# Kernel optimization log

Hardware: AMD Instinct MI355X
Metric: run time of the kernel (lower is better)

## Reference

```python
import jax, jax.numpy as jnp
import numpy as np

EPS_NORM = 1e-12  # torch F.normalize eps
CLAMP_MIN = 1e-6

def _l2_normalize(x, axis):
    n = jnp.sqrt(jnp.sum(x * x, axis=axis, keepdims=True))
    return x / jnp.maximum(n, EPS_NORM)

def setup_inputs() -> dict:
    key = jax.random.key(0)
    k1, k2 = jax.random.split(key)
    embedding = jax.random.normal(k1, (384,), dtype=jnp.float32)
    corpus_embeddings = jax.random.normal(k2, (1000000, 384), dtype=jnp.float32)
    return {"embedding": embedding, "corpus_embeddings": corpus_embeddings, "k": 5}

def reference(embedding, corpus_embeddings, k):
    # embedding: [d] -> [1, d]; corpus_embeddings: [N, d]
    e = embedding[None, :] if embedding.ndim == 1 else embedding
    e = _l2_normalize(e, axis=1)                      # [1, d]
    c = _l2_normalize(corpus_embeddings, axis=1)      # [N, d]
    # cosine_similarity of already-unit vectors == dot product (re-normalization
    # inside torch cosine_similarity is a no-op on unit vectors)
    sims = jnp.einsum('nd,d->n', c, e[0])             # [N]
    sims = jnp.maximum(sims, CLAMP_MIN)               # torch.clamp(min=1e-6)
    sims = jnp.nan_to_num(sims, nan=0.0)
    k = min(int(k), sims.shape[0])
    top_k_similarities, top_k_indices = jax.lax.top_k(sims, k)
    return top_k_similarities, top_k_indices
```

## Files before the change

### kernel.cpp

```cpp
#include <hip/hip_runtime.h>
#include <math.h>

#define NBLK 1024
#define K 5
#define D 384
#define D4 (D/4)
#define THREADS 256
#define GROUPS_PER_BLOCK (THREADS/16)
#define C1 (GROUPS_PER_BLOCK*K)
#define C2 (NBLK*K)

__device__ __forceinline__ bool better(float v1, int r1, float v2, int r2) {
    return (v1 > v2) || (v1 == v2 && r1 < r2);
}

__global__ void qnorm_kernel(const float* __restrict__ q, float* __restrict__ invq) {
    int l = threadIdx.x;
    float ss = 0.f;
    #pragma unroll
    for (int j = 0; j < 6; ++j) {
        float x = q[l + 64*j];
        ss += x * x;
    }
    #pragma unroll
    for (int m = 1; m < 64; m <<= 1) ss += __shfl_xor(ss, m);
    if (l == 0) invq[0] = 1.0f / fmaxf(sqrtf(ss), 1e-12f);
}

__global__ __launch_bounds__(THREADS) void sim_topk_kernel(
        const float* __restrict__ corpus, const float* __restrict__ q,
        const float* __restrict__ invq_p,
        float* __restrict__ bVals, int* __restrict__ bIdx, int N) {
    __shared__ float qs[D];
    float invq = invq_p[0];
    for (int i = threadIdx.x; i < D; i += THREADS) qs[i] = q[i] * invq;
    __syncthreads();
    const float4* q4 = reinterpret_cast<const float4*>(qs);

    const int lane16 = threadIdx.x & 15;
    const int group  = threadIdx.x >> 4;
    const int ggid   = blockIdx.x * GROUPS_PER_BLOCK + group;
    const int gcount = gridDim.x * GROUPS_PER_BLOCK;

    float tv[K]; int ti[K];
    #pragma unroll
    for (int i = 0; i < K; ++i) { tv[i] = -INFINITY; ti[i] = 0x7fffffff; }

    for (int row = ggid; row < N; row += gcount) {
        const float4* r4 = reinterpret_cast<const float4*>(corpus + (size_t)row * D);
        float dot = 0.f, nrm = 0.f;
        #pragma unroll
        for (int j = 0; j < 6; ++j) {
            float4 x = r4[lane16 + 16*j];
            float4 w = q4[lane16 + 16*j];
            dot += x.x*w.x + x.y*w.y + x.z*w.z + x.w*w.w;
            nrm += x.x*x.x + x.y*x.y + x.z*x.z + x.w*x.w;
        }
        #pragma unroll
        for (int m = 1; m < 16; m <<= 1) {
            dot += __shfl_xor(dot, m);
            nrm += __shfl_xor(nrm, m);
        }
        if (lane16 == 0) {
            float sim = dot / fmaxf(sqrtf(nrm), 1e-12f);
            sim = fmaxf(sim, 1e-6f);
            if (sim != sim) sim = 0.f;
            if (sim > tv[K-1]) {
                int j = K - 1;
                while (j > 0 && tv[j-1] < sim) { tv[j] = tv[j-1]; ti[j] = ti[j-1]; --j; }
                tv[j] = sim; ti[j] = row;
            }
        }
    }

    __shared__ float cv[C1]; __shared__ int ci[C1];
    __shared__ float rv[THREADS]; __shared__ int ri[THREADS]; __shared__ int rs[THREADS];
    if (lane16 == 0) {
        #pragma unroll
        for (int i = 0; i < K; ++i) { cv[group*K + i] = tv[i]; ci[group*K + i] = ti[i]; }
    }
    __syncthreads();

    for (int r = 0; r < K; ++r) {
        float bv = -INFINITY; int bi = 0x7fffffff; int bslot = -1;
        for (int c = threadIdx.x; c < C1; c += THREADS)
            if (better(cv[c], ci[c], bv, bi)) { bv = cv[c]; bi = ci[c]; bslot = c; }
        rv[threadIdx.x] = bv; ri[threadIdx.x] = bi; rs[threadIdx.x] = bslot;
        __syncthreads();
        for (int s = THREADS/2; s > 0; s >>= 1) {
            if (threadIdx.x < s) {
                if (better(rv[threadIdx.x+s], ri[threadIdx.x+s], rv[threadIdx.x], ri[threadIdx.x])) {
                    rv[threadIdx.x] = rv[threadIdx.x+s];
                    ri[threadIdx.x] = ri[threadIdx.x+s];
                    rs[threadIdx.x] = rs[threadIdx.x+s];
                }
            }
            __syncthreads();
        }
        if (threadIdx.x == 0) {
            bVals[blockIdx.x*K + r] = rv[0];
            bIdx [blockIdx.x*K + r] = ri[0];
            if (rs[0] >= 0) cv[rs[0]] = -INFINITY;
        }
        __syncthreads();
    }
}

__global__ __launch_bounds__(THREADS) void final_topk_kernel(
        const float* __restrict__ bVals, const int* __restrict__ bIdx,
        float* __restrict__ out, int nC) {
    __shared__ float cv[C2]; __shared__ int ci[C2];
    __shared__ float rv[THREADS]; __shared__ int ri[THREADS]; __shared__ int rs[THREADS];
    for (int c = threadIdx.x; c < nC; c += THREADS) { cv[c] = bVals[c]; ci[c] = bIdx[c]; }
    __syncthreads();

    for (int r = 0; r < K; ++r) {
        float bv = -INFINITY; int bi = 0x7fffffff; int bslot = -1;
        for (int c = threadIdx.x; c < nC; c += THREADS)
            if (better(cv[c], ci[c], bv, bi)) { bv = cv[c]; bi = ci[c]; bslot = c; }
        rv[threadIdx.x] = bv; ri[threadIdx.x] = bi; rs[threadIdx.x] = bslot;
        __syncthreads();
        for (int s = THREADS/2; s > 0; s >>= 1) {
            if (threadIdx.x < s) {
                if (better(rv[threadIdx.x+s], ri[threadIdx.x+s], rv[threadIdx.x], ri[threadIdx.x])) {
                    rv[threadIdx.x] = rv[threadIdx.x+s];
                    ri[threadIdx.x] = ri[threadIdx.x+s];
                    rs[threadIdx.x] = rs[threadIdx.x+s];
                }
            }
            __syncthreads();
        }
        if (threadIdx.x == 0) {
            out[r]     = rv[0];
            out[K + r] = (float)ri[0];
            if (rs[0] >= 0) cv[rs[0]] = -INFINITY;
        }
        __syncthreads();
    }
}

extern "C" void kernel_launch(void* const* d_in, const int* in_sizes, int n_in,
                              void* d_out, int out_size, void* d_ws, size_t ws_size,
                              hipStream_t stream) {
    const float* q      = (const float*)d_in[0];
    const float* corpus = (const float*)d_in[1];
    const int N = in_sizes[1] / D;

    char* ws = (char*)d_ws;
    float* invq  = (float*)ws;
    float* bVals = (float*)(ws + 256);
    int*   bIdx  = (int*)  (ws + 256 + NBLK*K*4);

    float* out = (float*)d_out;

    qnorm_kernel<<<1, 64, 0, stream>>>(q, invq);
    sim_topk_kernel<<<NBLK, THREADS, 0, stream>>>(corpus, q, invq, bVals, bIdx, N);
    final_topk_kernel<<<1, THREADS, 0, stream>>>(bVals, bIdx, out, NBLK*K);
}
```

Measured before the change: 289.8 us.

## Fuse query norm, similarity and final top-k into one kernel with last-block reduction

Result: slower. 513.6 us (+77.2%).

```diff
diff --git a/kernel.cpp b/kernel.cpp
--- a/kernel.cpp
+++ b/kernel.cpp
@@ -4,7 +4,6 @@
 #define NBLK 1024
 #define K 5
 #define D 384
-#define D4 (D/4)
 #define THREADS 256
 #define GROUPS_PER_BLOCK (THREADS/16)
 #define C1 (GROUPS_PER_BLOCK*K)
@@ -14,67 +13,107 @@
     return (v1 > v2) || (v1 == v2 && r1 < r2);
 }
 
-__global__ void qnorm_kernel(const float* __restrict__ q, float* __restrict__ invq) {
-    int l = threadIdx.x;
-    float ss = 0.f;
-    #pragma unroll
-    for (int j = 0; j < 6; ++j) {
-        float x = q[l + 64*j];
-        ss += x * x;
-    }
-    #pragma unroll
-    for (int m = 1; m < 64; m <<= 1) ss += __shfl_xor(ss, m);
-    if (l == 0) invq[0] = 1.0f / fmaxf(sqrtf(ss), 1e-12f);
-}
-
-__global__ __launch_bounds__(THREADS) void sim_topk_kernel(
+__global__ __launch_bounds__(THREADS) void fused_sim_topk_kernel(
         const float* __restrict__ corpus, const float* __restrict__ q,
-        const float* __restrict__ invq_p,
-        float* __restrict__ bVals, int* __restrict__ bIdx, int N) {
+        float* __restrict__ bVals, int* __restrict__ bIdx,
+        unsigned int* __restrict__ counter,
+        float* __restrict__ out, int N) {
     __shared__ float qs[D];
-    float invq = invq_p[0];
-    for (int i = threadIdx.x; i < D; i += THREADS) qs[i] = q[i] * invq;
-    __syncthreads();
-    const float4* q4 = reinterpret_cast<const float4*>(qs);
+    __shared__ float s_invq;
+    __shared__ float cv[C1]; __shared__ int ci[C1];
+    __shared__ float rv[THREADS]; __shared__ int ri[THREADS]; __shared__ int rs[THREADS];
+    __shared__ bool amLast;
+
+    float4* qs4 = (float4*)qs;
+    if (threadIdx.x < D/4) qs4[threadIdx.x] = ((const float4*)q)[threadIdx.x];
+    __syncthreads();
+    if (threadIdx.x < 64) {
+        float ss = 0.f;
+        #pragma unroll
+        for (int j = 0; j < 6; ++j) { float x = qs[threadIdx.x + 64*j]; ss += x*x; }
+        #pragma unroll
+        for (int m = 1; m < 64; m <<= 1) ss += __shfl_xor(ss, m);
+        if (threadIdx.x == 0) s_invq = 1.0f / fmaxf(sqrtf(ss), 1e-12f);
+    }
+    __syncthreads();
+    if (threadIdx.x < D/4) {
+        float iv = s_invq;
+        float4 v = qs4[threadIdx.x];
+        v.x *= iv; v.y *= iv; v.z *= iv; v.w *= iv;
+        qs4[threadIdx.x] = v;
+    }
+    __syncthreads();
+    const float4* q4 = (const float4*)qs;
 
     const int lane16 = threadIdx.x & 15;
     const int group  = threadIdx.x >> 4;
     const int ggid   = blockIdx.x * GROUPS_PER_BLOCK + group;
-    const int gcount = gridDim.x * GROUPS_PER_BLOCK;
+    const int gcount = NBLK * GROUPS_PER_BLOCK;
 
     float tv[K]; int ti[K];
     #pragma unroll
     for (int i = 0; i < K; ++i) { tv[i] = -INFINITY; ti[i] = 0x7fffffff; }
 
-    for (int row = ggid; row < N; row += gcount) {
-        const float4* r4 = reinterpret_cast<const float4*>(corpus + (size_t)row * D);
+    auto insert = [&](float sim, int r) {
+        if (sim > tv[K-1]) {
+            int j = K - 1;
+            while (j > 0 && tv[j-1] < sim) { tv[j] = tv[j-1]; ti[j] = ti[j-1]; --j; }
+            tv[j] = sim; ti[j] = r;
+        }
+    };
+
+    int row = ggid;
+    for (; row + gcount < N; row += 2*gcount) {
+        const int rowB = row + gcount;
+        const float4* rA = (const float4*)(corpus + (size_t)row  * D);
+        const float4* rB = (const float4*)(corpus + (size_t)rowB * D);
+        float dotA = 0.f, nrmA = 0.f, dotB = 0.f, nrmB = 0.f;
+        #pragma unroll
+        for (int j = 0; j < 6; ++j) {
+            float4 w  = q4[lane16 + 16*j];
+            float4 xA = rA[lane16 + 16*j];
+            float4 xB = rB[lane16 + 16*j];
+            dotA += xA.x*w.x + xA.y*w.y + xA.z*w.z + xA.w*w.w;
+            nrmA += xA.x*xA.x + xA.y*xA.y + xA.z*xA.z + xA.w*xA.w;
+            dotB += xB.x*w.x + xB.y*w.y + xB.z*w.z + xB.w*w.w;
+            nrmB += xB.x*xB.x + xB.y*xB.y + xB.z*xB.z + xB.w*xB.w;
+        }
+        #pragma unroll
+        for (int m = 1; m < 16; m <<= 1) {
+            dotA += __shfl_xor(dotA, m); nrmA += __shfl_xor(nrmA, m);
+            dotB += __shfl_xor(dotB, m); nrmB += __shfl_xor(nrmB, m);
+        }
+        if (lane16 == 0) {
+            float simA = dotA / fmaxf(sqrtf(nrmA), 1e-12f);
+            simA = fmaxf(simA, 1e-6f);
+            if (simA != simA) simA = 0.f;
+            insert(simA, row);
+            float simB = dotB / fmaxf(sqrtf(nrmB), 1e-12f);
+            simB = fmaxf(simB, 1e-6f);
+            if (simB != simB) simB = 0.f;
+            insert(simB, rowB);
+        }
+    }
+    if (row < N) {
+        const float4* rA = (const float4*)(corpus + (size_t)row * D);
         float dot = 0.f, nrm = 0.f;
         #pragma unroll
         for (int j = 0; j < 6; ++j) {
-            float4 x = r4[lane16 + 16*j];
             float4 w = q4[lane16 + 16*j];
+            float4 x = rA[lane16 + 16*j];
             dot += x.x*w.x + x.y*w.y + x.z*w.z + x.w*w.w;
             nrm += x.x*x.x + x.y*x.y + x.z*x.z + x.w*x.w;
         }
         #pragma unroll
-        for (int m = 1; m < 16; m <<= 1) {
-            dot += __shfl_xor(dot, m);
-            nrm += __shfl_xor(nrm, m);
-        }
+        for (int m = 1; m < 16; m <<= 1) { dot += __shfl_xor(dot, m); nrm += __shfl_xor(nrm, m); }
         if (lane16 == 0) {
             float sim = dot / fmaxf(sqrtf(nrm), 1e-12f);
             sim = fmaxf(sim, 1e-6f);
             if (sim != sim) sim = 0.f;
-            if (sim > tv[K-1]) {
-                int j = K - 1;
-                while (j > 0 && tv[j-1] < sim) { tv[j] = tv[j-1]; ti[j] = ti[j-1]; --j; }
-                tv[j] = sim; ti[j] = row;
-            }
-        }
-    }
-
-    __shared__ float cv[C1]; __shared__ int ci[C1];
-    __shared__ float rv[THREADS]; __shared__ int ri[THREADS]; __shared__ int rs[THREADS];
+            insert(sim, row);
+        }
+    }
+
     if (lane16 == 0) {
         #pragma unroll
         for (int i = 0; i < K; ++i) { cv[group*K + i] = tv[i]; ci[group*K + i] = ti[i]; }
@@ -104,20 +143,22 @@
         }
         __syncthreads();
     }
-}
-
-__global__ __launch_bounds__(THREADS) void final_topk_kernel(
-        const float* __restrict__ bVals, const int* __restrict__ bIdx,
-        float* __restrict__ out, int nC) {
-    __shared__ float cv[C2]; __shared__ int ci[C2];
-    __shared__ float rv[THREADS]; __shared__ int ri[THREADS]; __shared__ int rs[THREADS];
-    for (int c = threadIdx.x; c < nC; c += THREADS) { cv[c] = bVals[c]; ci[c] = bIdx[c]; }
-    __syncthreads();
+
+    __threadfence();
+    if (threadIdx.x == 0) {
+        unsigned int v = atomicAdd(counter, 1u);
+        amLast = (v == (unsigned int)(NBLK - 1));
+    }
+    __syncthreads();
+    if (!amLast) return;
+    __threadfence();
 
     for (int r = 0; r < K; ++r) {
         float bv = -INFINITY; int bi = 0x7fffffff; int bslot = -1;
-        for (int c = threadIdx.x; c < nC; c += THREADS)
-            if (better(cv[c], ci[c], bv, bi)) { bv = cv[c]; bi = ci[c]; bslot = c; }
+        for (int c = threadIdx.x; c < C2; c += THREADS) {
+            float v = bVals[c]; int idx = bIdx[c];
+            if (better(v, idx, bv, bi)) { bv = v; bi = idx; bslot = c; }
+        }
         rv[threadIdx.x] = bv; ri[threadIdx.x] = bi; rs[threadIdx.x] = bslot;
         __syncthreads();
         for (int s = THREADS/2; s > 0; s >>= 1) {
@@ -133,7 +174,8 @@
         if (threadIdx.x == 0) {
             out[r]     = rv[0];
             out[K + r] = (float)ri[0];
-            if (rs[0] >= 0) cv[rs[0]] = -INFINITY;
+            if (rs[0] >= 0) bVals[rs[0]] = -INFINITY;
+            __threadfence_block();
         }
         __syncthreads();
     }
@@ -147,13 +189,13 @@
     const int N = in_sizes[1] / D;
 
     char* ws = (char*)d_ws;
-    float* invq  = (float*)ws;
+    unsigned int* counter = (unsigned int*)ws;
     float* bVals = (float*)(ws + 256);
     int*   bIdx  = (int*)  (ws + 256 + NBLK*K*4);
 
     float* out = (float*)d_out;
 
-    qnorm_kernel<<<1, 64, 0, stream>>>(q, invq);
-    sim_topk_kernel<<<NBLK, THREADS, 0, stream>>>(corpus, q, invq, bVals, bIdx, N);
-    final_topk_kernel<<<1, THREADS, 0, stream>>>(bVals, bIdx, out, NBLK*K);
+    hipMemsetAsync(counter, 0, sizeof(unsigned int), stream);
+    fused_sim_topk_kernel<<<NBLK, THREADS, 0, stream>>>(
+        corpus, q, bVals, bIdx, counter, out, N);
 }
```
